# Performance work log

Measured on AMD Instinct MI355X. Metric: run time of the kernel, lower is better.

## Reference

```python
import jax, jax.numpy as jnp
import numpy as np

C = 512
NH = 8
HD = C // NH
GROUPS = 8
EPS = 1e-5

def group_norm(x, w, b):
    # x: [B,C,H,W], 8 groups
    B, Cc, H, W = x.shape
    xg = x.reshape(B, GROUPS, Cc // GROUPS, H, W)
    mu = xg.mean(axis=(2, 3, 4), keepdims=True)
    var = xg.var(axis=(2, 3, 4), keepdims=True)
    xn = (xg - mu) * jax.lax.rsqrt(var + EPS)
    xn = xn.reshape(B, Cc, H, W)
    return xn * w[None, :, None, None] + b[None, :, None, None]

def conv1x1(x, w, b):
    # w: [O,C], b: [O]
    return jnp.einsum('oc,bchw->bohw', w, x) + b[None, :, None, None]

def setup_inputs() -> dict:
    key = jax.random.key(0)
    ks = jax.random.split(key, 12)
    s = 1.0 / np.sqrt(C)
    inp = {
        'x': jax.random.normal(ks[0], (8, C, 32, 32), dtype=jnp.float32),
        'norm_w': jnp.ones((C,), jnp.float32),
        'norm_b': jnp.zeros((C,), jnp.float32),
        'qw': jax.random.uniform(ks[1], (C, C), jnp.float32, -s, s),
        'qb': jax.random.uniform(ks[2], (C,), jnp.float32, -s, s),
        'kw': jax.random.uniform(ks[3], (C, C), jnp.float32, -s, s),
        'kb': jax.random.uniform(ks[4], (C,), jnp.float32, -s, s),
        'vw': jax.random.uniform(ks[5], (C, C), jnp.float32, -s, s),
        'vb': jax.random.uniform(ks[6], (C,), jnp.float32, -s, s),
        'pw': jax.random.uniform(ks[7], (C, C), jnp.float32, -s, s),
        'pb': jax.random.uniform(ks[8], (C,), jnp.float32, -s, s),
    }
    return inp

def reference(x, norm_w, norm_b, qw, qb, kw, kb, vw, vb, pw, pb):
    b, c, h, w = x.shape
    scale = HD ** (-0.5)
    xn = group_norm(x, norm_w, norm_b)
    q = conv1x1(xn, qw, qb).reshape(b, NH, HD, h * w)
    k = conv1x1(xn, kw, kb).reshape(b, NH, HD, h * w)
    v = conv1x1(xn, vw, vb).reshape(b, NH, HD, h * w)
    attn = jnp.einsum('bhcn,bhcm->bhnm', q, k) * scale
    attn = jax.nn.softmax(attn, axis=-1)
    out = jnp.einsum('bhnm,bhcm->bhcn', attn, v)
    out = out.reshape(b, c, h, w)
    out = conv1x1(out, pw, pb)
    return out + x
```

## Files before the change

### kernel.cpp

```cpp
#include <hip/hip_runtime.h>

#define C_DIM 512
#define N_PIX 1024
#define B_DIM 8
#define NHEAD 8
#define HDIM 64
#define NGRP 8
#define CG 64
#define EPSF 1e-5f

typedef __bf16 bf16x8_t __attribute__((ext_vector_type(8)));
typedef __bf16 bf16x4_t __attribute__((ext_vector_type(4)));
typedef float  f32x4_t  __attribute__((ext_vector_type(4)));
typedef unsigned int u32x4_t __attribute__((ext_vector_type(4)));

__device__ __forceinline__ __bf16 f2b(float f) {
  unsigned int u = __builtin_bit_cast(unsigned int, f);
  u += 0x7fffu + ((u >> 16) & 1u);
  unsigned short s = (unsigned short)(u >> 16);
  return __builtin_bit_cast(__bf16, s);
}

__device__ __forceinline__ unsigned int pack_trunc(float a, float b) {
  return (__builtin_bit_cast(unsigned int, a) >> 16) |
         (__builtin_bit_cast(unsigned int, b) & 0xffff0000u);
}

__device__ __forceinline__ void async16(const void* g, void* l) {
  __builtin_amdgcn_global_load_lds((const __attribute__((address_space(1))) void*)g,
                                   (__attribute__((address_space(3))) void*)l, 16, 0, 0);
}

__global__ __launch_bounds__(256) void prep_kernel(
    const float* __restrict__ qw, const float* __restrict__ kw,
    const float* __restrict__ vw, const float* __restrict__ pw,
    __bf16* __restrict__ wb,
    const float* __restrict__ x, float2* __restrict__ psum)
{
  if (blockIdx.x < 1024) {
    int idx = blockIdx.x * 256 + threadIdx.x;
    int mat = idx >> 16;
    int off = (idx & 65535) * 4;
    const float* src = (mat == 0) ? qw : (mat == 1) ? kw : (mat == 2) ? vw : pw;
    float4 v = *(const float4*)(src + off);
    bf16x4_t pk;
    pk[0] = f2b(v.x); pk[1] = f2b(v.y); pk[2] = f2b(v.z); pk[3] = f2b(v.w);
    *(bf16x4_t*)(wb + mat * (512 * 512) + off) = pk;
  } else {
    const int t = blockIdx.x - 1024;
    const int s = t & 7, bg = t >> 3;
    const float* xp = x + ((size_t)bg * CG + s * 8) * N_PIX;
    float sum = 0.f, sum2 = 0.f;
#pragma unroll
    for (int it = 0; it < 8; it++) {
      float4 v = ((const float4*)xp)[it * 256 + threadIdx.x];
      sum  += v.x + v.y + v.z + v.w;
      sum2 += v.x * v.x + v.y * v.y + v.z * v.z + v.w * v.w;
    }
#pragma unroll
    for (int off = 32; off; off >>= 1) {
      sum  += __shfl_xor(sum, off, 64);
      sum2 += __shfl_xor(sum2, off, 64);
    }
    __shared__ float red[8];
    const int lane = threadIdx.x & 63, wv = threadIdx.x >> 6;
    if (lane == 0) { red[wv] = sum; red[4 + wv] = sum2; }
    __syncthreads();
    if (threadIdx.x == 0) {
      float s1 = red[0] + red[1] + red[2] + red[3];
      float s2 = red[4] + red[5] + red[6] + red[7];
      psum[bg * 8 + s] = make_float2(s1, s2);
    }
  }
}

__global__ __launch_bounds__(256) void gn_apply_kernel(
    const float* __restrict__ x, const float2* __restrict__ psum,
    const float* __restrict__ gw, const float* __restrict__ gb,
    __bf16* __restrict__ xnT)
{
  const int n0 = blockIdx.x * 32, b = blockIdx.y;
  const int tid = threadIdx.x;
  __shared__ float mu_s[8], rs_s[8];
  __shared__ __align__(16) __bf16 tile[32 * 520];

  if (tid < 8) {
    float s1 = 0.f, s2 = 0.f;
#pragma unroll
    for (int i = 0; i < 8; i++) {
      float2 p = psum[(b * 8 + tid) * 8 + i];
      s1 += p.x; s2 += p.y;
    }
    const float inv = 1.f / (float)(CG * N_PIX);
    float mu = s1 * inv;
    float var = s2 * inv - mu * mu;
    mu_s[tid] = mu;
    rs_s[tid] = rsqrtf(var + EPSF);
  }
  __syncthreads();

  const float* xb = x + (size_t)b * C_DIM * N_PIX + n0;
  const int cl = tid >> 3;
  const int nq = (tid & 7) * 4;
#pragma unroll
  for (int co = 0; co < 16; co++) {
    const int c = co * 32 + cl;
    float4 v = *(const float4*)(xb + (size_t)c * N_PIX + nq);
    const int g = c >> 6;
    const float rs = rs_s[g];
    const float a = rs * gw[c];
    const float bb = gb[c] - mu_s[g] * a;
    tile[(nq + 0) * 520 + c] = f2b(v.x * a + bb);
    tile[(nq + 1) * 520 + c] = f2b(v.y * a + bb);
    tile[(nq + 2) * 520 + c] = f2b(v.z * a + bb);
    tile[(nq + 3) * 520 + c] = f2b(v.w * a + bb);
  }
  __syncthreads();

  __bf16* dst = xnT + ((size_t)b * N_PIX + n0) * C_DIM;
  const int l32 = tid & 31, nr = tid >> 5;
#pragma unroll
  for (int no = 0; no < 4; no++) {
    const int n = no * 8 + nr;
#pragma unroll
    for (int co = 0; co < 2; co++) {
      const int c = co * 256 + l32 * 8;
      *(bf16x8_t*)(dst + (size_t)n * C_DIM + c) =
          *(const bf16x8_t*)(tile + n * 520 + c);
    }
  }
}

__device__ __forceinline__ void gemm_core_64(
    const __bf16* __restrict__ A, const __bf16* __restrict__ B,
    __bf16* As, __bf16* Bs, f32x4_t acc[2][4])
{
  const int tid  = threadIdx.x;
  const int lane = tid & 63;
  const int wv   = tid >> 6;
  const int quad = lane >> 4;
  const int l16  = lane & 15;
  const int wm = (wv >> 1) * 32;
  const int wn = (wv & 1) * 64;

  f32x4_t zero = {0.f, 0.f, 0.f, 0.f};
#pragma unroll
  for (int i = 0; i < 2; i++)
#pragma unroll
    for (int j = 0; j < 4; j++) acc[i][j] = zero;

  const int chA  = wv * 64 + lane;
  const int rA = chA >> 2,  kA = (chA & 3) * 8;
  const int chB0 = wv * 64 + lane, chB1 = 256 + wv * 64 + lane;
  const int rB0 = chB0 >> 2, kB0 = (chB0 & 3) * 8;
  const int rB1 = chB1 >> 2, kB1 = (chB1 & 3) * 8;

  async16(A + (size_t)rA * 512 + 0 + kA,  As + (wv * 64) * 8);
  async16(B + (size_t)rB0 * 512 + 0 + kB0, Bs + (wv * 64) * 8);
  async16(B + (size_t)rB1 * 512 + 0 + kB1, Bs + (256 + wv * 64) * 8);
  __builtin_amdgcn_s_waitcnt(0);
  __syncthreads();

  for (int kt2 = 0; kt2 < 8; kt2++) {
#pragma unroll
    for (int pp = 0; pp < 2; pp++) {
      const int pi = kt2 * 2 + pp;
      if (pi < 15) {
        const int kc = (pi + 1) * 32;
        const int nb = (pi + 1) & 1;
        async16(A + (size_t)rA * 512 + kc + kA,  As + nb * 2048 + (wv * 64) * 8);
        async16(B + (size_t)rB0 * 512 + kc + kB0, Bs + nb * 4096 + (wv * 64) * 8);
        async16(B + (size_t)rB1 * 512 + kc + kB1, Bs + nb * 4096 + (256 + wv * 64) * 8);
      }
      bf16x8_t af[2], bfr[4];
#pragma unroll
      for (int i = 0; i < 2; i++)
        af[i] = *(const bf16x8_t*)(As + pp * 2048 + (wm + i * 16 + l16) * 32 + quad * 8);
#pragma unroll
      for (int j = 0; j < 4; j++)
        bfr[j] = *(const bf16x8_t*)(Bs + pp * 4096 + (wn + j * 16 + l16) * 32 + quad * 8);
#pragma unroll
      for (int i = 0; i < 2; i++)
#pragma unroll
        for (int j = 0; j < 4; j++)
          acc[i][j] = __builtin_amdgcn_mfma_f32_16x16x32_bf16(af[i], bfr[j], acc[i][j], 0, 0, 0);
      __builtin_amdgcn_s_waitcnt(0);
      __syncthreads();
    }
  }
}

__global__ __launch_bounds__(256, 2) void gemm_qkv_kernel(
    const __bf16* __restrict__ wqkv, const float* __restrict__ qb,
    const float* __restrict__ kb, const float* __restrict__ vb,
    const __bf16* __restrict__ xnT,
    __bf16* __restrict__ qT, __bf16* __restrict__ kT, __bf16* __restrict__ vbuf)
{
  __shared__ __align__(16) __bf16 smem[20480];
  __bf16* Bs = smem + 12288;
  const int b = blockIdx.x;
  const int n0 = blockIdx.y * 128;
  const int m0 = blockIdx.z * 64;
  const __bf16* Aq = wqkv + (size_t)m0 * 512;
  const __bf16* Ak = Aq + 512 * 512;
  const __bf16* Av = Ak + 512 * 512;
  const __bf16* Bx = xnT + ((size_t)b * N_PIX + n0) * 512;

  const int tid = threadIdx.x, lane = tid & 63, wv = tid >> 6;
  const int quad = lane >> 4, l16 = lane & 15;
  const int wm = (wv >> 1) * 32, wn = (wv & 1) * 64;

  const f32x4_t zero = {0.f, 0.f, 0.f, 0.f};
  f32x4_t acc[3][2][4];
#pragma unroll
  for (int m = 0; m < 3; m++)
#pragma unroll
    for (int i = 0; i < 2; i++)
#pragma unroll
      for (int j = 0; j < 4; j++) acc[m][i][j] = zero;

  const int chA = wv * 64 + lane;
  const int rA = chA >> 2, kA = (chA & 3) * 8;
  const int chB0 = wv * 64 + lane, chB1 = 256 + wv * 64 + lane;
  const int rB0 = chB0 >> 2, kB0 = (chB0 & 3) * 8;
  const int rB1 = chB1 >> 2, kB1 = (chB1 & 3) * 8;

  async16(Aq + (size_t)rA * 512 + kA, smem + (wv * 64) * 8);
  async16(Ak + (size_t)rA * 512 + kA, smem + 4096 + (wv * 64) * 8);
  async16(Av + (size_t)rA * 512 + kA, smem + 8192 + (wv * 64) * 8);
  async16(Bx + (size_t)rB0 * 512 + kB0, Bs + (wv * 64) * 8);
  async16(Bx + (size_t)rB1 * 512 + kB1, Bs + (256 + wv * 64) * 8);
  __builtin_amdgcn_s_waitcnt(0);
  __syncthreads();

  for (int kt2 = 0; kt2 < 8; kt2++) {
#pragma unroll
    for (int pp = 0; pp < 2; pp++) {
      const int pi = kt2 * 2 + pp;
      if (pi < 15) {
        const int kc = (pi + 1) * 32;
        const int nb = (pi + 1) & 1;
        async16(Aq + (size_t)rA * 512 + kc + kA, smem + nb * 2048 + (wv * 64) * 8);
        async16(Ak + (size_t)rA * 512 + kc + kA, smem + 4096 + nb * 2048 + (wv * 64) * 8);
        async16(Av + (size_t)rA * 512 + kc + kA, smem + 8192 + nb * 2048 + (wv * 64) * 8);
        async16(Bx + (size_t)rB0 * 512 + kc + kB0, Bs + nb * 4096 + (wv * 64) * 8);
        async16(Bx + (size_t)rB1 * 512 + kc + kB1, Bs + nb * 4096 + (256 + wv * 64) * 8);
      }
      bf16x8_t bfr[4];
#pragma unroll
      for (int j = 0; j < 4; j++)
        bfr[j] = *(const bf16x8_t*)(Bs + pp * 4096 + (wn + j * 16 + l16) * 32 + quad * 8);
#pragma unroll
      for (int m = 0; m < 3; m++) {
        bf16x8_t af[2];
#pragma unroll
        for (int i = 0; i < 2; i++)
          af[i] = *(const bf16x8_t*)(smem + m * 4096 + pp * 2048 + (wm + i * 16 + l16) * 32 + quad * 8);
#pragma unroll
        for (int i = 0; i < 2; i++)
#pragma unroll
          for (int j = 0; j < 4; j++)
            acc[m][i][j] = __builtin_amdgcn_mfma_f32_16x16x32_bf16(af[i], bfr[j], acc[m][i][j], 0, 0, 0);
      }
      __builtin_amdgcn_s_waitcnt(0);
      __syncthreads();
    }
  }

  const float qscale = 0.125f * 1.44269504f;
#pragma unroll
  for (int mat = 0; mat < 2; mat++) {
    const float* bias = (mat == 0) ? qb : kb;
    const float sc = (mat == 0) ? qscale : 1.0f;
    __bf16* dst = (mat == 0) ? qT : kT;
#pragma unroll
    for (int i = 0; i < 2; i++) {
      const int crow = wm + i * 16 + quad * 4;
      const int o = m0 + crow;
      float b0 = bias[o], b1 = bias[o + 1], b2 = bias[o + 2], b3 = bias[o + 3];
#pragma unroll
      for (int j = 0; j < 4; j++) {
        const int nl = wn + j * 16 + l16;
        bf16x4_t pk;
        pk[0] = f2b((acc[mat][i][j][0] + b0) * sc);
        pk[1] = f2b((acc[mat][i][j][1] + b1) * sc);
        pk[2] = f2b((acc[mat][i][j][2] + b2) * sc);
        pk[3] = f2b((acc[mat][i][j][3] + b3) * sc);
        *(bf16x4_t*)(smem + nl * 72 + crow) = pk;
      }
    }
    __syncthreads();
#pragma unroll
    for (int it = 0; it < 4; it++) {
      const int n = it * 32 + (tid >> 3);
      const int c = (tid & 7) * 8;
      *(bf16x8_t*)(dst + ((size_t)b * N_PIX + n0 + n) * 512 + m0 + c) =
          *(const bf16x8_t*)(smem + n * 72 + c);
    }
    __syncthreads();
  }
#pragma unroll
  for (int i = 0; i < 2; i++) {
    const int crow = wm + i * 16 + quad * 4;
    const int o = m0 + crow;
    float b0 = vb[o], b1 = vb[o + 1], b2 = vb[o + 2], b3 = vb[o + 3];
#pragma unroll
    for (int j = 0; j < 4; j++) {
      const int nl = wn + j * 16 + l16;
      smem[(crow + 0) * 132 + nl] = f2b(acc[2][i][j][0] + b0);
      smem[(crow + 1) * 132 + nl] = f2b(acc[2][i][j][1] + b1);
      smem[(crow + 2) * 132 + nl] = f2b(acc[2][i][j][2] + b2);
      smem[(crow + 3) * 132 + nl] = f2b(acc[2][i][j][3] + b3);
    }
  }
  __syncthreads();
  {
    const int c = tid >> 2;
    const int nch = (tid & 3) * 32;
    __bf16* vd = vbuf + ((size_t)b * 512 + m0 + c) * N_PIX + n0 + nch;
#pragma unroll
    for (int k = 0; k < 4; k++)
      *(bf16x8_t*)(vd + k * 8) = *(const bf16x8_t*)(smem + c * 132 + nch + k * 8);
  }
}

__global__ __launch_bounds__(256, 2) void attn_kernel(
    const __bf16* __restrict__ qT, const __bf16* __restrict__ kT,
    const __bf16* __restrict__ vbuf, __bf16* __restrict__ aT)
{
  __shared__ __align__(16) __bf16 Ks[2][64 * 72];
  __shared__ __align__(16) __bf16 Vp[2][64 * 72];
  const int bh = blockIdx.x;
  const int b = bh >> 3, head = bh & 7;
  const int n0 = blockIdx.y * 128;
  const int tid = threadIdx.x, lane = tid & 63, wv = tid >> 6;
  const int quad = lane >> 4, l16 = lane & 15;

  bf16x8_t qf[2][2];
#pragma unroll
  for (int qt = 0; qt < 2; qt++) {
    const __bf16* qp = qT + ((size_t)b * N_PIX + n0 + wv * 32 + qt * 16 + l16) * 512 + head * 64;
    qf[qt][0] = *(const bf16x8_t*)(qp + quad * 8);
    qf[qt][1] = *(const bf16x8_t*)(qp + 32 + quad * 8);
  }

  const __bf16* kp = kT + ((size_t)b * N_PIX) * 512 + head * 64;
  const __bf16* vp = vbuf + ((size_t)b * 512 + head * 64) * N_PIX;

  const int srow = tid >> 2, scol = (tid & 3) * 16;
  const int pr0 = scol >> 5, hh0 = (scol >> 4) & 1;
  const int pos0 = pr0 * 32 + ((scol >> 2) & 3) * 8 + hh0 * 4;
  const int mc1 = scol + 8;
  const int pr1 = mc1 >> 5, hh1 = (mc1 >> 4) & 1;
  const int pos1 = pr1 * 32 + ((mc1 >> 2) & 3) * 8 + hh1 * 4;

  bf16x8_t kreg0 = *(const bf16x8_t*)(kp + (size_t)srow * 512 + scol);
  bf16x8_t kreg1 = *(const bf16x8_t*)(kp + (size_t)srow * 512 + scol + 8);
  bf16x8_t vreg0 = *(const bf16x8_t*)(vp + (size_t)srow * N_PIX + scol);
  bf16x8_t vreg1 = *(const bf16x8_t*)(vp + (size_t)srow * N_PIX + scol + 8);
  {
    *(bf16x8_t*)(Ks[0] + srow * 72 + scol)     = kreg0;
    *(bf16x8_t*)(Ks[0] + srow * 72 + scol + 8) = kreg1;
    bf16x4_t lo, hi;
#pragma unroll
    for (int r = 0; r < 4; r++) { lo[r] = vreg0[r]; hi[r] = vreg0[4 + r]; }
    *(bf16x4_t*)(Vp[0] + srow * 72 + pos0)     = lo;
    *(bf16x4_t*)(Vp[0] + srow * 72 + pos0 + 8) = hi;
#pragma unroll
    for (int r = 0; r < 4; r++) { lo[r] = vreg1[r]; hi[r] = vreg1[4 + r]; }
    *(bf16x4_t*)(Vp[0] + srow * 72 + pos1)     = lo;
    *(bf16x4_t*)(Vp[0] + srow * 72 + pos1 + 8) = hi;
  }
  kreg0 = *(const bf16x8_t*)(kp + (size_t)(64 + srow) * 512 + scol);
  kreg1 = *(const bf16x8_t*)(kp + (size_t)(64 + srow) * 512 + scol + 8);
  vreg0 = *(const bf16x8_t*)(vp + (size_t)srow * N_PIX + 64 + scol);
  vreg1 = *(const bf16x8_t*)(vp + (size_t)srow * N_PIX + 64 + scol + 8);
  __syncthreads();

  const f32x4_t zero = {0.f, 0.f, 0.f, 0.f};
  f32x4_t oacc[2][4];
#pragma unroll
  for (int qt = 0; qt < 2; qt++)
#pragma unroll
    for (int jc = 0; jc < 4; jc++) oacc[qt][jc] = zero;
  f32x4_t lsum4[2] = {zero, zero};

  for (int mt = 0; mt < 16; mt++) {
    const int cur = mt & 1, nxt = cur ^ 1;
    const __bf16* Kc = Ks[cur];
    const __bf16* Vc = Vp[cur];

    f32x4_t sacc[2][4];
    __builtin_amdgcn_s_setprio(1);
#pragma unroll
    for (int mb = 0; mb < 4; mb++) {
      bf16x8_t kf0 = *(const bf16x8_t*)(Kc + (mb * 16 + l16) * 72 + quad * 8);
      bf16x8_t kf1 = *(const bf16x8_t*)(Kc + (mb * 16 + l16) * 72 + 32 + quad * 8);
#pragma unroll
      for (int qt = 0; qt < 2; qt++) {
        f32x4_t s = zero;
        s = __builtin_amdgcn_mfma_f32_16x16x32_bf16(kf0, qf[qt][0], s, 0, 0, 0);
        s = __builtin_amdgcn_mfma_f32_16x16x32_bf16(kf1, qf[qt][1], s, 0, 0, 0);
        sacc[qt][mb] = s;
      }
    }
    __builtin_amdgcn_s_setprio(0);

    bf16x8_t pf[2][2];
#pragma unroll
    for (int qt = 0; qt < 2; qt++) {
      float p[4][4];
#pragma unroll
      for (int mb = 0; mb < 4; mb++)
#pragma unroll
        for (int r = 0; r < 4; r++) {
          p[mb][r] = __builtin_amdgcn_exp2f(sacc[qt][mb][r]);
          lsum4[qt][r] += p[mb][r];
        }
#pragma unroll
      for (int pr = 0; pr < 2; pr++) {
        u32x4_t u;
        u[0] = pack_trunc(p[2 * pr][0],     p[2 * pr][1]);
        u[1] = pack_trunc(p[2 * pr][2],     p[2 * pr][3]);
        u[2] = pack_trunc(p[2 * pr + 1][0], p[2 * pr + 1][1]);
        u[3] = pack_trunc(p[2 * pr + 1][2], p[2 * pr + 1][3]);
        pf[qt][pr] = __builtin_bit_cast(bf16x8_t, u);
      }
    }

    __builtin_amdgcn_s_setprio(1);
#pragma unroll
    for (int jc = 0; jc < 4; jc++) {
      const int vrow = (jc * 16 + l16) * 72;
#pragma unroll
      for (int pr = 0; pr < 2; pr++) {
        bf16x8_t vf = *(const bf16x8_t*)(Vc + vrow + pr * 32 + quad * 8);
#pragma unroll
        for (int qt = 0; qt < 2; qt++)
          oacc[qt][jc] = __builtin_amdgcn_mfma_f32_16x16x32_bf16(vf, pf[qt][pr], oacc[qt][jc], 0, 0, 0);
      }
    }
    __builtin_amdgcn_s_setprio(0);

    if (mt < 15) {
      *(bf16x8_t*)(Ks[nxt] + srow * 72 + scol)     = kreg0;
      *(bf16x8_t*)(Ks[nxt] + srow * 72 + scol + 8) = kreg1;
      bf16x4_t lo, hi;
#pragma unroll
      for (int r = 0; r < 4; r++) { lo[r] = vreg0[r]; hi[r] = vreg0[4 + r]; }
      *(bf16x4_t*)(Vp[nxt] + srow * 72 + pos0)     = lo;
      *(bf16x4_t*)(Vp[nxt] + srow * 72 + pos0 + 8) = hi;
#pragma unroll
      for (int r = 0; r < 4; r++) { lo[r] = vreg1[r]; hi[r] = vreg1[4 + r]; }
      *(bf16x4_t*)(Vp[nxt] + srow * 72 + pos1)     = lo;
      *(bf16x4_t*)(Vp[nxt] + srow * 72 + pos1 + 8) = hi;
      if (mt < 14) {
        kreg0 = *(const bf16x8_t*)(kp + (size_t)((mt + 2) * 64 + srow) * 512 + scol);
        kreg1 = *(const bf16x8_t*)(kp + (size_t)((mt + 2) * 64 + srow) * 512 + scol + 8);
        vreg0 = *(const bf16x8_t*)(vp + (size_t)srow * N_PIX + (mt + 2) * 64 + scol);
        vreg1 = *(const bf16x8_t*)(vp + (size_t)srow * N_PIX + (mt + 2) * 64 + scol + 8);
      }
      __syncthreads();
    }
  }

  __syncthreads();
  __bf16* Tr = &Ks[0][0];
#pragma unroll
  for (int qt = 0; qt < 2; qt++) {
    float lsum = lsum4[qt][0] + lsum4[qt][1] + lsum4[qt][2] + lsum4[qt][3];
    lsum += __shfl_xor(lsum, 16, 64);
    lsum += __shfl_xor(lsum, 32, 64);
    const float inv = 1.f / lsum;
    const int nl = wv * 32 + qt * 16 + l16;
#pragma unroll
    for (int jc = 0; jc < 4; jc++) {
      bf16x4_t o4;
#pragma unroll
      for (int r = 0; r < 4; r++) o4[r] = f2b(oacc[qt][jc][r] * inv);
      *(bf16x4_t*)(Tr + nl * 72 + jc * 16 + quad * 4) = o4;
    }
  }
  __syncthreads();
#pragma unroll
  for (int it = 0; it < 4; it++) {
    const int n = it * 32 + (tid >> 3);
    const int c = (tid & 7) * 8;
    *(bf16x8_t*)(aT + ((size_t)b * N_PIX + n0 + n) * 512 + head * 64 + c) =
        *(const bf16x8_t*)(Tr + n * 72 + c);
  }
}

__global__ __launch_bounds__(256, 4) void gemm_proj_kernel(
    const __bf16* __restrict__ wp, const float* __restrict__ pb,
    const __bf16* __restrict__ aT, const float* __restrict__ x,
    float* __restrict__ out)
{
  __shared__ __align__(16) __bf16 smem[12288];
  __bf16* As = smem;
  __bf16* Bs = smem + 4096;
  const int b = blockIdx.x;
  const int n0 = blockIdx.y * 128;
  const int m0 = blockIdx.z * 64;
  const __bf16* A = wp + (size_t)m0 * 512;
  const __bf16* B = aT + ((size_t)b * N_PIX + n0) * 512;
  f32x4_t acc[2][4];
  gemm_core_64(A, B, As, Bs, acc);
  const int tid = threadIdx.x, lane = tid & 63, wv = tid >> 6;
  const int quad = lane >> 4, l16 = lane & 15;
  const int wm = (wv >> 1) * 32, wn = (wv & 1) * 64;
#pragma unroll
  for (int i = 0; i < 2; i++) {
    const int o = m0 + wm + i * 16 + quad * 4;
#pragma unroll
    for (int j = 0; j < 4; j++) {
      const int n = n0 + wn + j * 16 + l16;
#pragma unroll
      for (int r = 0; r < 4; r++) {
        size_t idx = ((size_t)b * 512 + o + r) * N_PIX + n;
        out[idx] = acc[i][j][r] + pb[o + r] + x[idx];
      }
    }
  }
}

extern "C" void kernel_launch(void* const* d_in, const int* in_sizes, int n_in,
                              void* d_out, int out_size, void* d_ws, size_t ws_size,
                              hipStream_t stream)
{
  (void)in_sizes; (void)n_in; (void)out_size; (void)ws_size;
  const float* x   = (const float*)d_in[0];
  const float* gnw = (const float*)d_in[1];
  const float* gnb = (const float*)d_in[2];
  const float* qw  = (const float*)d_in[3];
  const float* qb  = (const float*)d_in[4];
  const float* kw  = (const float*)d_in[5];
  const float* kb  = (const float*)d_in[6];
  const float* vw  = (const float*)d_in[7];
  const float* vb  = (const float*)d_in[8];
  const float* pw  = (const float*)d_in[9];
  const float* pb  = (const float*)d_in[10];
  float* out = (float*)d_out;

  char* ws = (char*)d_ws;
  __bf16* wb   = (__bf16*)(ws);
  __bf16* xnT  = (__bf16*)(ws + (size_t)(2  << 20));
  __bf16* qTb  = (__bf16*)(ws + (size_t)(10 << 20));
  __bf16* kTb  = (__bf16*)(ws + (size_t)(18 << 20));
  __bf16* vbf  = (__bf16*)(ws + (size_t)(26 << 20));
  __bf16* aT   = (__bf16*)(ws + (size_t)(34 << 20));
  float2* psum = (float2*)(ws + (size_t)(42 << 20));

  hipLaunchKernelGGL(prep_kernel, dim3(1536), dim3(256), 0, stream,
                     qw, kw, vw, pw, wb, x, psum);
  hipLaunchKernelGGL(gn_apply_kernel, dim3(32, 8), dim3(256), 0, stream, x, psum, gnw, gnb, xnT);
  hipLaunchKernelGGL(gemm_qkv_kernel, dim3(8, 8, 8), dim3(256), 0, stream,
                     wb, qb, kb, vb, xnT, qTb, kTb, vbf);
  hipLaunchKernelGGL(attn_kernel, dim3(64, 8), dim3(256), 0, stream, qTb, kTb, vbf, aT);
  hipLaunchKernelGGL(gemm_proj_kernel, dim3(8, 8, 8), dim3(256), 0, stream,
                     wb + (size_t)3 * 512 * 512, pb, aT, x, out);
}
```

Measured before the change: 148.2 us.

## Use partial vmcnt waits and raw barriers in GEMM loops, split GN apply grid

The GEMM main loops now wait with vmcnt(N) so only the current stage's async loads must land, which keeps the next prefetch in flight across the barrier. Raw s_barrier and sched_barrier replace __syncthreads, and setprio is raised around the MFMA blocks. The attention kernel waits only on LDS counters before its barriers, and the group-norm apply kernel splits channels over a z grid dimension for more blocks and less shared memory per block. This relies on the hand-counted vmcnt values being exact; a wrong count would allow reads of shared memory before the data arrives.

```diff
diff --git a/kernel.cpp b/kernel.cpp
--- a/kernel.cpp
+++ b/kernel.cpp
@@ -79,10 +79,10 @@
     const float* __restrict__ gw, const float* __restrict__ gb,
     __bf16* __restrict__ xnT)
 {
-  const int n0 = blockIdx.x * 32, b = blockIdx.y;
+  const int n0 = blockIdx.x * 32, b = blockIdx.y, z = blockIdx.z;
   const int tid = threadIdx.x;
   __shared__ float mu_s[8], rs_s[8];
-  __shared__ __align__(16) __bf16 tile[32 * 520];
+  __shared__ __align__(16) __bf16 tile[32 * 264];
 
   if (tid < 8) {
     float s1 = 0.f, s2 = 0.f;
@@ -103,31 +103,29 @@
   const int cl = tid >> 3;
   const int nq = (tid & 7) * 4;
 #pragma unroll
-  for (int co = 0; co < 16; co++) {
-    const int c = co * 32 + cl;
+  for (int co = 0; co < 8; co++) {
+    const int cc = co * 32 + cl;
+    const int c = z * 256 + cc;
     float4 v = *(const float4*)(xb + (size_t)c * N_PIX + nq);
     const int g = c >> 6;
     const float rs = rs_s[g];
     const float a = rs * gw[c];
     const float bb = gb[c] - mu_s[g] * a;
-    tile[(nq + 0) * 520 + c] = f2b(v.x * a + bb);
-    tile[(nq + 1) * 520 + c] = f2b(v.y * a + bb);
-    tile[(nq + 2) * 520 + c] = f2b(v.z * a + bb);
-    tile[(nq + 3) * 520 + c] = f2b(v.w * a + bb);
+    tile[(nq + 0) * 264 + cc] = f2b(v.x * a + bb);
+    tile[(nq + 1) * 264 + cc] = f2b(v.y * a + bb);
+    tile[(nq + 2) * 264 + cc] = f2b(v.z * a + bb);
+    tile[(nq + 3) * 264 + cc] = f2b(v.w * a + bb);
   }
   __syncthreads();
 
-  __bf16* dst = xnT + ((size_t)b * N_PIX + n0) * C_DIM;
+  __bf16* dst = xnT + ((size_t)b * N_PIX + n0) * C_DIM + z * 256;
   const int l32 = tid & 31, nr = tid >> 5;
 #pragma unroll
   for (int no = 0; no < 4; no++) {
     const int n = no * 8 + nr;
-#pragma unroll
-    for (int co = 0; co < 2; co++) {
-      const int c = co * 256 + l32 * 8;
-      *(bf16x8_t*)(dst + (size_t)n * C_DIM + c) =
-          *(const bf16x8_t*)(tile + n * 520 + c);
-    }
+    const int cc = l32 * 8;
+    *(bf16x8_t*)(dst + (size_t)n * C_DIM + cc) =
+        *(const bf16x8_t*)(tile + n * 264 + cc);
   }
 }
 
@@ -155,11 +153,9 @@
   const int rB0 = chB0 >> 2, kB0 = (chB0 & 3) * 8;
   const int rB1 = chB1 >> 2, kB1 = (chB1 & 3) * 8;
 
-  async16(A + (size_t)rA * 512 + 0 + kA,  As + (wv * 64) * 8);
-  async16(B + (size_t)rB0 * 512 + 0 + kB0, Bs + (wv * 64) * 8);
-  async16(B + (size_t)rB1 * 512 + 0 + kB1, Bs + (256 + wv * 64) * 8);
-  __builtin_amdgcn_s_waitcnt(0);
-  __syncthreads();
+  async16(A + (size_t)rA * 512 + kA,  As + (wv * 64) * 8);
+  async16(B + (size_t)rB0 * 512 + kB0, Bs + (wv * 64) * 8);
+  async16(B + (size_t)rB1 * 512 + kB1, Bs + (256 + wv * 64) * 8);
 
   for (int kt2 = 0; kt2 < 8; kt2++) {
 #pragma unroll
@@ -171,7 +167,12 @@
         async16(A + (size_t)rA * 512 + kc + kA,  As + nb * 2048 + (wv * 64) * 8);
         async16(B + (size_t)rB0 * 512 + kc + kB0, Bs + nb * 4096 + (wv * 64) * 8);
         async16(B + (size_t)rB1 * 512 + kc + kB1, Bs + nb * 4096 + (256 + wv * 64) * 8);
-      }
+        asm volatile("s_waitcnt vmcnt(3)" ::: "memory");
+      } else {
+        asm volatile("s_waitcnt vmcnt(0)" ::: "memory");
+      }
+      __builtin_amdgcn_s_barrier();
+      __builtin_amdgcn_sched_barrier(0);
       bf16x8_t af[2], bfr[4];
 #pragma unroll
       for (int i = 0; i < 2; i++)
@@ -179,13 +180,15 @@
 #pragma unroll
       for (int j = 0; j < 4; j++)
         bfr[j] = *(const bf16x8_t*)(Bs + pp * 4096 + (wn + j * 16 + l16) * 32 + quad * 8);
+      __builtin_amdgcn_s_setprio(1);
 #pragma unroll
       for (int i = 0; i < 2; i++)
 #pragma unroll
         for (int j = 0; j < 4; j++)
           acc[i][j] = __builtin_amdgcn_mfma_f32_16x16x32_bf16(af[i], bfr[j], acc[i][j], 0, 0, 0);
-      __builtin_amdgcn_s_waitcnt(0);
-      __syncthreads();
+      __builtin_amdgcn_s_setprio(0);
+      __builtin_amdgcn_sched_barrier(0);
+      __builtin_amdgcn_s_barrier();
     }
   }
 }
@@ -230,8 +233,6 @@
   async16(Av + (size_t)rA * 512 + kA, smem + 8192 + (wv * 64) * 8);
   async16(Bx + (size_t)rB0 * 512 + kB0, Bs + (wv * 64) * 8);
   async16(Bx + (size_t)rB1 * 512 + kB1, Bs + (256 + wv * 64) * 8);
-  __builtin_amdgcn_s_waitcnt(0);
-  __syncthreads();
 
   for (int kt2 = 0; kt2 < 8; kt2++) {
 #pragma unroll
@@ -245,7 +246,12 @@
         async16(Av + (size_t)rA * 512 + kc + kA, smem + 8192 + nb * 2048 + (wv * 64) * 8);
         async16(Bx + (size_t)rB0 * 512 + kc + kB0, Bs + nb * 4096 + (wv * 64) * 8);
         async16(Bx + (size_t)rB1 * 512 + kc + kB1, Bs + nb * 4096 + (256 + wv * 64) * 8);
-      }
+        asm volatile("s_waitcnt vmcnt(5)" ::: "memory");
+      } else {
+        asm volatile("s_waitcnt vmcnt(0)" ::: "memory");
+      }
+      __builtin_amdgcn_s_barrier();
+      __builtin_amdgcn_sched_barrier(0);
       bf16x8_t bfr[4];
 #pragma unroll
       for (int j = 0; j < 4; j++)
@@ -256,14 +262,16 @@
 #pragma unroll
         for (int i = 0; i < 2; i++)
           af[i] = *(const bf16x8_t*)(smem + m * 4096 + pp * 2048 + (wm + i * 16 + l16) * 32 + quad * 8);
+        __builtin_amdgcn_s_setprio(1);
 #pragma unroll
         for (int i = 0; i < 2; i++)
 #pragma unroll
           for (int j = 0; j < 4; j++)
             acc[m][i][j] = __builtin_amdgcn_mfma_f32_16x16x32_bf16(af[i], bfr[j], acc[m][i][j], 0, 0, 0);
-      }
-      __builtin_amdgcn_s_waitcnt(0);
-      __syncthreads();
+        __builtin_amdgcn_s_setprio(0);
+      }
+      __builtin_amdgcn_sched_barrier(0);
+      __builtin_amdgcn_s_barrier();
     }
   }
 
@@ -375,7 +383,9 @@
   kreg1 = *(const bf16x8_t*)(kp + (size_t)(64 + srow) * 512 + scol + 8);
   vreg0 = *(const bf16x8_t*)(vp + (size_t)srow * N_PIX + 64 + scol);
   vreg1 = *(const bf16x8_t*)(vp + (size_t)srow * N_PIX + 64 + scol + 8);
-  __syncthreads();
+  asm volatile("s_waitcnt lgkmcnt(0)" ::: "memory");
+  __builtin_amdgcn_s_barrier();
+  __builtin_amdgcn_sched_barrier(0);
 
   const f32x4_t zero = {0.f, 0.f, 0.f, 0.f};
   f32x4_t oacc[2][4];
@@ -460,7 +470,9 @@
         vreg0 = *(const bf16x8_t*)(vp + (size_t)srow * N_PIX + (mt + 2) * 64 + scol);
         vreg1 = *(const bf16x8_t*)(vp + (size_t)srow * N_PIX + (mt + 2) * 64 + scol + 8);
       }
-      __syncthreads();
+      asm volatile("s_waitcnt lgkmcnt(0)" ::: "memory");
+      __builtin_amdgcn_s_barrier();
+      __builtin_amdgcn_sched_barrier(0);
     }
   }
 
@@ -553,7 +565,7 @@
 
   hipLaunchKernelGGL(prep_kernel, dim3(1536), dim3(256), 0, stream,
                      qw, kw, vw, pw, wb, x, psum);
-  hipLaunchKernelGGL(gn_apply_kernel, dim3(32, 8), dim3(256), 0, stream, x, psum, gnw, gnb, xnT);
+  hipLaunchKernelGGL(gn_apply_kernel, dim3(32, 8, 2), dim3(256), 0, stream, x, psum, gnw, gnb, xnT);
   hipLaunchKernelGGL(gemm_qkv_kernel, dim3(8, 8, 8), dim3(256), 0, stream,
                      wb, qb, kb, vb, xnT, qTb, kTb, vbf);
   hipLaunchKernelGGL(attn_kernel, dim3(64, 8), dim3(256), 0, stream, qTb, kTb, vbf, aT);
```

New measurement: 149.5 us. Within noise of the previous version (+0.9%).
